# Optimization experiments

Hardware: AMD Instinct MI355X
Metric: run time of the kernel (lower is better)

The kernel has to match this reference:

```python
import jax, jax.numpy as jnp
import numpy as np

B, N, M, D, H = 2, 4096, 4096, 512, 8
P = D // H


def setup_inputs() -> dict:
    key = jax.random.key(0)
    ks = jax.random.split(key, 9)
    s = 1.0 / np.sqrt(D)
    return {
        "queries": jax.random.normal(ks[0], (B, N, D), dtype=jnp.float32),
        "keys": jax.random.normal(ks[1], (B, M, D), dtype=jnp.float32),
        "values": jax.random.normal(ks[2], (B, M, D), dtype=jnp.float32),
        "Wq": jax.random.normal(ks[3], (D, D), dtype=jnp.float32) * s,
        "bq": jax.random.normal(ks[4], (D,), dtype=jnp.float32) * s,
        "Wk": jax.random.normal(ks[5], (D, D), dtype=jnp.float32) * s,
        "bk": jax.random.normal(ks[6], (D,), dtype=jnp.float32) * s,
        "Wv": jax.random.normal(ks[7], (D, D), dtype=jnp.float32) * s,
        "bv": jax.random.normal(ks[8], (D,), dtype=jnp.float32) * s,
    }


def reference(queries, keys, values, Wq, bq, Wk, bk, Wv, bv):
    b, n, d = queries.shape
    m = keys.shape[1]
    h, p = H, D // H
    temperature = jnp.asarray(p, queries.dtype) ** 0.5
    # Linear projections (torch Linear: x @ W^T + b; here W stored as [in, out])
    q = (queries @ Wq + bq).reshape(b, n, h, p)
    k = (keys @ Wk + bk).reshape(b, m, h, p)
    v = (values @ Wv + bv).reshape(b, m, h, p)
    # scaled dot-product attention per head; scores [b, h, n, m]
    scores = jnp.einsum("bnhp,bmhp->bhnm", q, k) / temperature
    attn = jax.nn.softmax(scores, axis=-1)
    out = jnp.einsum("bhnm,bmhp->bnhp", attn, v)
    return out.reshape(b, n, d)
```

## Files before the change

### kernel.cpp

```cpp
#include <hip/hip_runtime.h>
#include <stdint.h>

#define B_ 2
#define N_ 4096
#define M_ 4096
#define D_ 512
#define H_ 8
#define P_ 64

typedef short bf16x8 __attribute__((ext_vector_type(8)));
typedef float f32x4 __attribute__((ext_vector_type(4)));
typedef unsigned short u16;
typedef unsigned int u32;
typedef u32 u32x4 __attribute__((ext_vector_type(4)));

static __device__ __forceinline__ u16 f2bf(float f) {
  u32 u = __builtin_bit_cast(u32, f);
  u32 r = u + 0x7fffu + ((u >> 16) & 1u);
  return (u16)(r >> 16);
}

static __device__ __forceinline__ u32 cvtpk(float lo, float hi_) {
  u32 d;
  asm("v_cvt_pk_bf16_f32 %0, %1, %2" : "=v"(d) : "v"(lo), "v"(hi_));
  return d;
}

static __device__ __forceinline__ float fexp2(float x) {
  float r;
  asm("v_exp_f32 %0, %1" : "=v"(r) : "v"(x));
  return r;
}

static __device__ __forceinline__ u32 permpk(const bf16x8& a0, const bf16x8& a1, int i) {
  u32x4 a0w = __builtin_bit_cast(u32x4, a0);
  u32x4 a1w = __builtin_bit_cast(u32x4, a1);
  int wd = i >> 1;
  u32 sel = (i & 1) ? 0x07060302u : 0x05040100u;
  return __builtin_amdgcn_perm(a1w[wd], a0w[wd], sel);
}

__global__ __launch_bounds__(256) void wt_kernel(const float* __restrict__ Wq,
                                                 const float* __restrict__ Wk,
                                                 const float* __restrict__ Wv,
                                                 u16* __restrict__ Wt) {
  __shared__ float tile[32][33];
  int z = blockIdx.z;
  const float* W = (z == 0) ? Wq : (z == 1) ? Wk : Wv;
  u16* out = Wt + (size_t)z * D_ * D_;
  int o0 = blockIdx.x * 32, d0 = blockIdx.y * 32;
  int tx = threadIdx.x, ty = threadIdx.y;
#pragma unroll
  for (int k = 0; k < 4; k++) tile[ty + k * 8][tx] = W[(size_t)(d0 + ty + k * 8) * D_ + o0 + tx];
  __syncthreads();
#pragma unroll
  for (int k = 0; k < 4; k++) out[(size_t)(o0 + ty + k * 8) * D_ + d0 + tx] = f2bf(tile[tx][ty + k * 8]);
}

__global__ __launch_bounds__(256) void proj_kernel(const float* __restrict__ Xq,
                                                   const float* __restrict__ Xk,
                                                   const float* __restrict__ Xv,
                                                   const u16* __restrict__ Wt,
                                                   const float* __restrict__ bq,
                                                   const float* __restrict__ bk,
                                                   const float* __restrict__ bv,
                                                   u16* __restrict__ QKV) {
  int z = blockIdx.z;
  const float* X = (z == 0) ? Xq : (z == 1) ? Xk : Xv;
  const float* bias = (z == 0) ? bq : (z == 1) ? bk : bv;
  const u16* W = Wt + (size_t)z * D_ * D_;
  u16* Y = QKV + (size_t)z * (B_ * N_ * D_);
  const float scale = (z == 0) ? 0.18033688011112042f : 1.0f;

  __shared__ u16 Alds[128 * 32];
  __shared__ u16 Blds[128 * 32];

  int t = threadIdx.x;
  int lane = t & 63, w = t >> 6;
  int wm = w >> 1, wn = w & 1;
  int l15 = lane & 15, g = lane >> 4;
  int rb = blockIdx.y * 128, ob = blockIdx.x * 128;

  const f32x4 zero4 = {0.f, 0.f, 0.f, 0.f};
  f32x4 acc[4][4];
#pragma unroll
  for (int m = 0; m < 4; m++)
#pragma unroll
    for (int n = 0; n < 4; n++) acc[m][n] = zero4;

  for (int kb = 0; kb < D_; kb += 32) {
    __syncthreads();
#pragma unroll
    for (int i = 0; i < 4; i++) {
      int chunk = t + i * 256;
      int row = chunk >> 3, c4 = chunk & 7;
      const float4 v = *(const float4*)&X[(size_t)(rb + row) * D_ + kb + c4 * 4];
      u32 lo = (u32)f2bf(v.x) | ((u32)f2bf(v.y) << 16);
      u32 hi = (u32)f2bf(v.z) | ((u32)f2bf(v.w) << 16);
      int byte = row * 64 + ((c4 * 8) ^ ((row & 3) << 4));
      uint2 d;
      d.x = lo;
      d.y = hi;
      *(uint2*)((char*)Alds + byte) = d;
    }
#pragma unroll
    for (int i = 0; i < 2; i++) {
      int chunk = t + i * 256;
      int row = chunk >> 2, c = chunk & 3;
      bf16x8 v = *(const bf16x8*)&W[(size_t)(ob + row) * D_ + kb + c * 8];
      int byte = row * 64 + ((c * 16) ^ ((row & 3) << 4));
      *(bf16x8*)((char*)Blds + byte) = v;
    }
    __syncthreads();

    bf16x8 a[4], b[4];
#pragma unroll
    for (int m = 0; m < 4; m++) {
      int row = wm * 64 + m * 16 + l15;
      int byte = row * 64 + ((g * 16) ^ ((row & 3) << 4));
      a[m] = *(const bf16x8*)((char*)Alds + byte);
    }
#pragma unroll
    for (int n = 0; n < 4; n++) {
      int row = wn * 64 + n * 16 + l15;
      int byte = row * 64 + ((g * 16) ^ ((row & 3) << 4));
      b[n] = *(const bf16x8*)((char*)Blds + byte);
    }
#pragma unroll
    for (int m = 0; m < 4; m++)
#pragma unroll
      for (int n = 0; n < 4; n++)
        acc[m][n] = __builtin_amdgcn_mfma_f32_16x16x32_bf16(a[m], b[n], acc[m][n], 0, 0, 0);
  }

#pragma unroll
  for (int n = 0; n < 4; n++) {
    int col = ob + wn * 64 + n * 16 + l15;
    float bv_ = bias[col];
#pragma unroll
    for (int m = 0; m < 4; m++) {
      int row0 = rb + wm * 64 + m * 16 + g * 4;
#pragma unroll
      for (int r = 0; r < 4; r++) {
        float y = (acc[m][n][r] + bv_) * scale;
        Y[(size_t)(row0 + r) * D_ + col] = f2bf(y);
      }
    }
  }
}

__global__ __launch_bounds__(256, 2) void attn_kernel(const u16* __restrict__ QKV,
                                                      float* __restrict__ out) {
  const u16* Q = QKV;
  const u16* K = QKV + (size_t)(B_ * N_ * D_);
  const u16* V = K + (size_t)(B_ * N_ * D_);

  __shared__ u16 Klds[2][128 * 64];
  __shared__ u16 Vlds[2][2][64 * 64];

  char* KL = (char*)&Klds[0][0];
  char* VL = (char*)&Vlds[0][0][0];

  int t = threadIdx.x, l = t & 63, w = t >> 6;
  int l15 = l & 15, g = (l >> 4) & 3;
  int swz = (l15 & 7) << 4;

  int bid = blockIdx.x + 32 * (blockIdx.y + 8 * blockIdx.z);
  int sbid = (bid & 7) * 64 + (bid >> 3);
  int qt = sbid & 31, h = (sbid >> 5) & 7, b = sbid >> 8;
  int qwa = qt * 128 + w * 16;
  int qwb = qwa + 64;

  const u16* Kb = K + (size_t)(b * M_) * D_ + h * P_;
  const u16* Vb = V + (size_t)(b * M_) * D_ + h * P_;

  bf16x8 qfa[2], qfb[2];
  const u16* qrow_a = Q + (size_t)(b * N_ + qwa + l15) * D_ + h * P_;
  const u16* qrow_b = Q + (size_t)(b * N_ + qwb + l15) * D_ + h * P_;
#pragma unroll
  for (int step = 0; step < 2; step++) {
    qfa[step] = *(const bf16x8*)(qrow_a + step * 32 + g * 8);
    qfb[step] = *(const bf16x8*)(qrow_b + step * 32 + g * 8);
  }

  int koff0 = l15 * 128 + ((g * 16) ^ swz);
  int koff1 = l15 * 128 + ((64 + g * 16) ^ swz);
  int voff0 = koff0, voff1 = koff1;
  int krow = t >> 3, kc = t & 7;
  int kwoff = krow * 128 + ((kc * 16) ^ ((krow & 7) << 4));
  const u16* kg = Kb + (size_t)krow * D_ + kc * 8;
  int kp = t & 31, p0 = (t >> 5) * 8;
  int kv0 = 2 * kp, blk = kv0 >> 5, ww_ = kv0 & 31;
  int slot = blk * 32 + ((ww_ >> 2) & 3) * 8 + ((ww_ >> 4) << 2) + (ww_ & 3);
  int vwB = p0 * 128 + 2 * slot;
  const u16* vg0 = Vb + (size_t)kv0 * D_ + p0;
  const u16* vg1 = vg0 + D_;

  const f32x4 zc = {0.f, 0.f, 0.f, 0.f};
  const u32x4 onesw = {0x3F803F80u, 0x3F803F80u, 0x3F803F80u, 0x3F803F80u};
  const bf16x8 ones_f = __builtin_bit_cast(bf16x8, onesw);
  f32x4 oa[4], ob_[4], ol_a = zc, ol_b = zc;
#pragma unroll
  for (int i = 0; i < 4; i++) {
    oa[i] = zc;
    ob_[i] = zc;
  }

  {
#pragma unroll
    for (int i = 0; i < 4; i++)
      *(bf16x8*)(KL + kwoff + i * 4096) = *(const bf16x8*)(kg + (size_t)(32 * i) * D_);
    bf16x8 a0 = *(const bf16x8*)vg0;
    bf16x8 a1 = *(const bf16x8*)vg1;
    bf16x8 c0 = *(const bf16x8*)(vg0 + (size_t)64 * D_);
    bf16x8 c1 = *(const bf16x8*)(vg1 + (size_t)64 * D_);
#pragma unroll
    for (int i = 0; i < 8; i++) {
      int off = (vwB ^ (i << 4)) + i * 128;
      *(u32*)(VL + off) = permpk(a0, a1, i);
      *(u32*)(VL + off + 8192) = permpk(c0, c1, i);
    }
  }
  kwoff ^= 0x4000;
  vwB ^= 0x4000;
  const u16* kgp = kg + (size_t)128 * D_;
  const u16* vgp0 = vg0 + (size_t)128 * D_;
  const u16* vgp1 = vg1 + (size_t)128 * D_;
  __syncthreads();

  const int NT = M_ / 128;
  for (int kt = 0; kt < NT; kt++) {
    bf16x8 kn0 = {}, kn1 = {}, kn2 = {}, kn3 = {}, vnA0 = {}, vnA1 = {}, vnB0 = {}, vnB1 = {};
    if (kt + 1 < NT) {
      kn0 = *(const bf16x8*)kgp;
      kn1 = *(const bf16x8*)(kgp + (size_t)32 * D_);
      kn2 = *(const bf16x8*)(kgp + (size_t)64 * D_);
      kn3 = *(const bf16x8*)(kgp + (size_t)96 * D_);
      vnA0 = *(const bf16x8*)vgp0;
      vnA1 = *(const bf16x8*)vgp1;
      vnB0 = *(const bf16x8*)(vgp0 + (size_t)64 * D_);
      vnB1 = *(const bf16x8*)(vgp1 + (size_t)64 * D_);
      kgp += (size_t)128 * D_;
      vgp0 += (size_t)128 * D_;
      vgp1 += (size_t)128 * D_;
    }

#pragma unroll
    for (int hh = 0; hh < 2; hh++) {
      const int hb = hh * 8192;

      f32x4 sa[4], sb[4];
      __builtin_amdgcn_s_setprio(1);
#pragma unroll
      for (int tt = 0; tt < 4; tt++) {
        bf16x8 kf0 = *(const bf16x8*)(KL + koff0 + hb + tt * 2048);
        sa[tt] = __builtin_amdgcn_mfma_f32_16x16x32_bf16(kf0, qfa[0], zc, 0, 0, 0);
        sb[tt] = __builtin_amdgcn_mfma_f32_16x16x32_bf16(kf0, qfb[0], zc, 0, 0, 0);
        bf16x8 kf1 = *(const bf16x8*)(KL + koff1 + hb + tt * 2048);
        sa[tt] = __builtin_amdgcn_mfma_f32_16x16x32_bf16(kf1, qfa[1], sa[tt], 0, 0, 0);
        sb[tt] = __builtin_amdgcn_mfma_f32_16x16x32_bf16(kf1, qfb[1], sb[tt], 0, 0, 0);
      }
      __builtin_amdgcn_s_setprio(0);

#pragma unroll
      for (int tt = 0; tt < 4; tt++)
#pragma unroll
        for (int r = 0; r < 4; r++) {
          sa[tt][r] = fexp2(sa[tt][r]);
          sb[tt][r] = fexp2(sb[tt][r]);
        }

      u32 pwa[2][4], pwb[2][4];
#pragma unroll
      for (int kb2 = 0; kb2 < 2; kb2++)
#pragma unroll
        for (int wd = 0; wd < 4; wd++) {
          const f32x4& sva = sa[2 * kb2 + (wd >> 1)];
          const f32x4& svb = sb[2 * kb2 + (wd >> 1)];
          pwa[kb2][wd] = cvtpk(sva[(wd & 1) * 2], sva[(wd & 1) * 2 + 1]);
          pwb[kb2][wd] = cvtpk(svb[(wd & 1) * 2], svb[(wd & 1) * 2 + 1]);
        }

      __builtin_amdgcn_s_setprio(1);
#pragma unroll
      for (int kb2 = 0; kb2 < 2; kb2++) {
        u32x4 pva = {pwa[kb2][0], pwa[kb2][1], pwa[kb2][2], pwa[kb2][3]};
        u32x4 pvb = {pwb[kb2][0], pwb[kb2][1], pwb[kb2][2], pwb[kb2][3]};
        bf16x8 pfa = __builtin_bit_cast(bf16x8, pva);
        bf16x8 pfb = __builtin_bit_cast(bf16x8, pvb);
        int voff = (kb2 ? voff1 : voff0) + hb;
#pragma unroll
        for (int tt = 0; tt < 4; tt++) {
          bf16x8 vf = *(const bf16x8*)(VL + voff + tt * 2048);
          oa[tt] = __builtin_amdgcn_mfma_f32_16x16x32_bf16(vf, pfa, oa[tt], 0, 0, 0);
          ob_[tt] = __builtin_amdgcn_mfma_f32_16x16x32_bf16(vf, pfb, ob_[tt], 0, 0, 0);
        }
        ol_a = __builtin_amdgcn_mfma_f32_16x16x32_bf16(ones_f, pfa, ol_a, 0, 0, 0);
        ol_b = __builtin_amdgcn_mfma_f32_16x16x32_bf16(ones_f, pfb, ol_b, 0, 0, 0);
      }
      __builtin_amdgcn_s_setprio(0);
    }

    if (kt + 1 < NT) {
      *(bf16x8*)(KL + kwoff) = kn0;
      *(bf16x8*)(KL + kwoff + 4096) = kn1;
      *(bf16x8*)(KL + kwoff + 8192) = kn2;
      *(bf16x8*)(KL + kwoff + 12288) = kn3;
#pragma unroll
      for (int i = 0; i < 8; i++) {
        int off = (vwB ^ (i << 4)) + i * 128;
        *(u32*)(VL + off) = permpk(vnA0, vnA1, i);
        *(u32*)(VL + off + 8192) = permpk(vnB0, vnB1, i);
      }
    }
    koff0 ^= 0x4000;
    koff1 ^= 0x4000;
    voff0 ^= 0x4000;
    voff1 ^= 0x4000;
    kwoff ^= 0x4000;
    vwB ^= 0x4000;
    __syncthreads();
  }

  float rla = 1.0f / ol_a[0], rlb = 1.0f / ol_b[0];
  float* orow_a = out + (size_t)(b * N_ + qwa + l15) * D_ + h * P_;
  float* orow_b = out + (size_t)(b * N_ + qwb + l15) * D_ + h * P_;
#pragma unroll
  for (int tt = 0; tt < 4; tt++) {
    float4 sta = {oa[tt][0] * rla, oa[tt][1] * rla, oa[tt][2] * rla, oa[tt][3] * rla};
    *(float4*)(orow_a + tt * 16 + g * 4) = sta;
    float4 stb = {ob_[tt][0] * rlb, ob_[tt][1] * rlb, ob_[tt][2] * rlb, ob_[tt][3] * rlb};
    *(float4*)(orow_b + tt * 16 + g * 4) = stb;
  }
}

extern "C" void kernel_launch(void* const* d_in, const int* in_sizes, int n_in,
                              void* d_out, int out_size, void* d_ws, size_t ws_size,
                              hipStream_t stream) {
  const float* queries = (const float*)d_in[0];
  const float* keys = (const float*)d_in[1];
  const float* values = (const float*)d_in[2];
  const float* Wq = (const float*)d_in[3];
  const float* bq = (const float*)d_in[4];
  const float* Wk = (const float*)d_in[5];
  const float* bk = (const float*)d_in[6];
  const float* Wv = (const float*)d_in[7];
  const float* bv = (const float*)d_in[8];
  float* out = (float*)d_out;

  u16* QKV = (u16*)d_ws;
  u16* Wt = QKV + (size_t)3 * B_ * N_ * D_;

  wt_kernel<<<dim3(16, 16, 3), dim3(32, 8), 0, stream>>>(Wq, Wk, Wv, Wt);
  proj_kernel<<<dim3(4, 64, 3), 256, 0, stream>>>(queries, keys, values, Wt, bq, bk, bv, QKV);
  attn_kernel<<<dim3(32, 8, 2), 256, 0, stream>>>(QKV, out);
}
```

Before: 120.8 us.

## Double attention query tile to 256 rows with 512-thread blocks sharing K/V tiles

The attention kernel now runs 8 waves per block over 256 query rows, so each staged 128-key K/V tile in LDS serves twice as many queries. Each thread loads half as many K/V vectors per iteration, which cuts global and LDS-staging traffic per query. The inner loop also computes scores for both 64-key halves before the exp and PV stages, giving the scheduler more independent MFMA work. The costs are higher register pressure under the tighter (512,2) launch bound, which could cause spills, and a grid half as large (256 blocks).

```diff
diff --git a/kernel.cpp b/kernel.cpp
--- a/kernel.cpp
+++ b/kernel.cpp
@@ -149,7 +149,7 @@
   }
 }
 
-__global__ __launch_bounds__(256, 2) void attn_kernel(const u16* __restrict__ QKV,
+__global__ __launch_bounds__(512, 2) void attn_kernel(const u16* __restrict__ QKV,
                                                       float* __restrict__ out) {
   const u16* Q = QKV;
   const u16* K = QKV + (size_t)(B_ * N_ * D_);
@@ -165,11 +165,11 @@
   int l15 = l & 15, g = (l >> 4) & 3;
   int swz = (l15 & 7) << 4;
 
-  int bid = blockIdx.x + 32 * (blockIdx.y + 8 * blockIdx.z);
-  int sbid = (bid & 7) * 64 + (bid >> 3);
-  int qt = sbid & 31, h = (sbid >> 5) & 7, b = sbid >> 8;
-  int qwa = qt * 128 + w * 16;
-  int qwb = qwa + 64;
+  int bid = blockIdx.x + 16 * (blockIdx.y + 8 * blockIdx.z);
+  int sbid = (bid & 7) * 32 + (bid >> 3);
+  int qt = sbid & 15, h = (sbid >> 4) & 7, b = sbid >> 7;
+  int qwa = qt * 256 + w * 16;
+  int qwb = qwa + 128;
 
   const u16* Kb = K + (size_t)(b * M_) * D_ + h * P_;
   const u16* Vb = V + (size_t)(b * M_) * D_ + h * P_;
@@ -186,14 +186,17 @@
   int koff0 = l15 * 128 + ((g * 16) ^ swz);
   int koff1 = l15 * 128 + ((64 + g * 16) ^ swz);
   int voff0 = koff0, voff1 = koff1;
+
   int krow = t >> 3, kc = t & 7;
   int kwoff = krow * 128 + ((kc * 16) ^ ((krow & 7) << 4));
-  const u16* kg = Kb + (size_t)krow * D_ + kc * 8;
-  int kp = t & 31, p0 = (t >> 5) * 8;
-  int kv0 = 2 * kp, blk = kv0 >> 5, ww_ = kv0 & 31;
-  int slot = blk * 32 + ((ww_ >> 2) & 3) * 8 + ((ww_ >> 4) << 2) + (ww_ & 3);
-  int vwB = p0 * 128 + 2 * slot;
-  const u16* vg0 = Vb + (size_t)kv0 * D_ + p0;
+  const u16* kg0 = Kb + (size_t)krow * D_ + kc * 8;
+  const u16* kg1 = kg0 + (size_t)64 * D_;
+  int hv = t >> 8, th = t & 255;
+  int kp = th & 31, p0 = (th >> 5) * 8;
+  int kv0 = 2 * kp, blk2 = kv0 >> 5, ww_ = kv0 & 31;
+  int slot = blk2 * 32 + ((ww_ >> 2) & 3) * 8 + ((ww_ >> 4) << 2) + (ww_ & 3);
+  int vwB = hv * 0x2000 + p0 * 128 + 2 * slot;
+  const u16* vg0 = Vb + (size_t)(hv * 64 + kv0) * D_ + p0;
   const u16* vg1 = vg0 + D_;
 
   const f32x4 zc = {0.f, 0.f, 0.f, 0.f};
@@ -207,111 +210,137 @@
   }
 
   {
-#pragma unroll
-    for (int i = 0; i < 4; i++)
-      *(bf16x8*)(KL + kwoff + i * 4096) = *(const bf16x8*)(kg + (size_t)(32 * i) * D_);
+    *(bf16x8*)(KL + kwoff) = *(const bf16x8*)kg0;
+    *(bf16x8*)(KL + kwoff + 8192) = *(const bf16x8*)kg1;
     bf16x8 a0 = *(const bf16x8*)vg0;
     bf16x8 a1 = *(const bf16x8*)vg1;
-    bf16x8 c0 = *(const bf16x8*)(vg0 + (size_t)64 * D_);
-    bf16x8 c1 = *(const bf16x8*)(vg1 + (size_t)64 * D_);
-#pragma unroll
-    for (int i = 0; i < 8; i++) {
-      int off = (vwB ^ (i << 4)) + i * 128;
-      *(u32*)(VL + off) = permpk(a0, a1, i);
-      *(u32*)(VL + off + 8192) = permpk(c0, c1, i);
-    }
+#pragma unroll
+    for (int i = 0; i < 8; i++) *(u32*)(VL + ((vwB ^ (i << 4)) + i * 128)) = permpk(a0, a1, i);
   }
   kwoff ^= 0x4000;
   vwB ^= 0x4000;
-  const u16* kgp = kg + (size_t)128 * D_;
+  const u16* kgp0 = kg0 + (size_t)128 * D_;
+  const u16* kgp1 = kg1 + (size_t)128 * D_;
   const u16* vgp0 = vg0 + (size_t)128 * D_;
   const u16* vgp1 = vg1 + (size_t)128 * D_;
   __syncthreads();
 
   const int NT = M_ / 128;
   for (int kt = 0; kt < NT; kt++) {
-    bf16x8 kn0 = {}, kn1 = {}, kn2 = {}, kn3 = {}, vnA0 = {}, vnA1 = {}, vnB0 = {}, vnB1 = {};
+    bf16x8 kn0 = {}, kn1 = {}, vn0 = {}, vn1 = {};
     if (kt + 1 < NT) {
-      kn0 = *(const bf16x8*)kgp;
-      kn1 = *(const bf16x8*)(kgp + (size_t)32 * D_);
-      kn2 = *(const bf16x8*)(kgp + (size_t)64 * D_);
-      kn3 = *(const bf16x8*)(kgp + (size_t)96 * D_);
-      vnA0 = *(const bf16x8*)vgp0;
-      vnA1 = *(const bf16x8*)vgp1;
-      vnB0 = *(const bf16x8*)(vgp0 + (size_t)64 * D_);
-      vnB1 = *(const bf16x8*)(vgp1 + (size_t)64 * D_);
-      kgp += (size_t)128 * D_;
+      kn0 = *(const bf16x8*)kgp0;
+      kn1 = *(const bf16x8*)kgp1;
+      vn0 = *(const bf16x8*)vgp0;
+      vn1 = *(const bf16x8*)vgp1;
+      kgp0 += (size_t)128 * D_;
+      kgp1 += (size_t)128 * D_;
       vgp0 += (size_t)128 * D_;
       vgp1 += (size_t)128 * D_;
     }
 
-#pragma unroll
-    for (int hh = 0; hh < 2; hh++) {
-      const int hb = hh * 8192;
-
-      f32x4 sa[4], sb[4];
-      __builtin_amdgcn_s_setprio(1);
+    f32x4 sa0[4], sb0[4], sa1[4], sb1[4];
+
+    __builtin_amdgcn_s_setprio(1);
+#pragma unroll
+    for (int tt = 0; tt < 4; tt++) {
+      bf16x8 kf0 = *(const bf16x8*)(KL + koff0 + tt * 2048);
+      sa0[tt] = __builtin_amdgcn_mfma_f32_16x16x32_bf16(kf0, qfa[0], zc, 0, 0, 0);
+      sb0[tt] = __builtin_amdgcn_mfma_f32_16x16x32_bf16(kf0, qfb[0], zc, 0, 0, 0);
+      bf16x8 kf1 = *(const bf16x8*)(KL + koff1 + tt * 2048);
+      sa0[tt] = __builtin_amdgcn_mfma_f32_16x16x32_bf16(kf1, qfa[1], sa0[tt], 0, 0, 0);
+      sb0[tt] = __builtin_amdgcn_mfma_f32_16x16x32_bf16(kf1, qfb[1], sb0[tt], 0, 0, 0);
+    }
+#pragma unroll
+    for (int tt = 0; tt < 4; tt++) {
+      bf16x8 kf0 = *(const bf16x8*)(KL + koff0 + 8192 + tt * 2048);
+      sa1[tt] = __builtin_amdgcn_mfma_f32_16x16x32_bf16(kf0, qfa[0], zc, 0, 0, 0);
+      sb1[tt] = __builtin_amdgcn_mfma_f32_16x16x32_bf16(kf0, qfb[0], zc, 0, 0, 0);
+      bf16x8 kf1 = *(const bf16x8*)(KL + koff1 + 8192 + tt * 2048);
+      sa1[tt] = __builtin_amdgcn_mfma_f32_16x16x32_bf16(kf1, qfa[1], sa1[tt], 0, 0, 0);
+      sb1[tt] = __builtin_amdgcn_mfma_f32_16x16x32_bf16(kf1, qfb[1], sb1[tt], 0, 0, 0);
+    }
+    __builtin_amdgcn_s_setprio(0);
+
+    u32 pwa0[2][4], pwb0[2][4];
+#pragma unroll
+    for (int tt = 0; tt < 4; tt++)
+#pragma unroll
+      for (int r = 0; r < 4; r++) {
+        sa0[tt][r] = fexp2(sa0[tt][r]);
+        sb0[tt][r] = fexp2(sb0[tt][r]);
+      }
+#pragma unroll
+    for (int kb2 = 0; kb2 < 2; kb2++)
+#pragma unroll
+      for (int wd = 0; wd < 4; wd++) {
+        const f32x4& sva = sa0[2 * kb2 + (wd >> 1)];
+        const f32x4& svb = sb0[2 * kb2 + (wd >> 1)];
+        pwa0[kb2][wd] = cvtpk(sva[(wd & 1) * 2], sva[(wd & 1) * 2 + 1]);
+        pwb0[kb2][wd] = cvtpk(svb[(wd & 1) * 2], svb[(wd & 1) * 2 + 1]);
+      }
+
+    __builtin_amdgcn_s_setprio(1);
+#pragma unroll
+    for (int kb2 = 0; kb2 < 2; kb2++) {
+      u32x4 pva = {pwa0[kb2][0], pwa0[kb2][1], pwa0[kb2][2], pwa0[kb2][3]};
+      u32x4 pvb = {pwb0[kb2][0], pwb0[kb2][1], pwb0[kb2][2], pwb0[kb2][3]};
+      bf16x8 pfa = __builtin_bit_cast(bf16x8, pva);
+      bf16x8 pfb = __builtin_bit_cast(bf16x8, pvb);
+      int voff = kb2 ? voff1 : voff0;
 #pragma unroll
       for (int tt = 0; tt < 4; tt++) {
-        bf16x8 kf0 = *(const bf16x8*)(KL + koff0 + hb + tt * 2048);
-        sa[tt] = __builtin_amdgcn_mfma_f32_16x16x32_bf16(kf0, qfa[0], zc, 0, 0, 0);
-        sb[tt] = __builtin_amdgcn_mfma_f32_16x16x32_bf16(kf0, qfb[0], zc, 0, 0, 0);
-        bf16x8 kf1 = *(const bf16x8*)(KL + koff1 + hb + tt * 2048);
-        sa[tt] = __builtin_amdgcn_mfma_f32_16x16x32_bf16(kf1, qfa[1], sa[tt], 0, 0, 0);
-        sb[tt] = __builtin_amdgcn_mfma_f32_16x16x32_bf16(kf1, qfb[1], sb[tt], 0, 0, 0);
-      }
-      __builtin_amdgcn_s_setprio(0);
-
-#pragma unroll
-      for (int tt = 0; tt < 4; tt++)
-#pragma unroll
-        for (int r = 0; r < 4; r++) {
-          sa[tt][r] = fexp2(sa[tt][r]);
-          sb[tt][r] = fexp2(sb[tt][r]);
-        }
-
-      u32 pwa[2][4], pwb[2][4];
-#pragma unroll
-      for (int kb2 = 0; kb2 < 2; kb2++)
-#pragma unroll
-        for (int wd = 0; wd < 4; wd++) {
-          const f32x4& sva = sa[2 * kb2 + (wd >> 1)];
-          const f32x4& svb = sb[2 * kb2 + (wd >> 1)];
-          pwa[kb2][wd] = cvtpk(sva[(wd & 1) * 2], sva[(wd & 1) * 2 + 1]);
-          pwb[kb2][wd] = cvtpk(svb[(wd & 1) * 2], svb[(wd & 1) * 2 + 1]);
-        }
-
-      __builtin_amdgcn_s_setprio(1);
-#pragma unroll
-      for (int kb2 = 0; kb2 < 2; kb2++) {
-        u32x4 pva = {pwa[kb2][0], pwa[kb2][1], pwa[kb2][2], pwa[kb2][3]};
-        u32x4 pvb = {pwb[kb2][0], pwb[kb2][1], pwb[kb2][2], pwb[kb2][3]};
-        bf16x8 pfa = __builtin_bit_cast(bf16x8, pva);
-        bf16x8 pfb = __builtin_bit_cast(bf16x8, pvb);
-        int voff = (kb2 ? voff1 : voff0) + hb;
-#pragma unroll
-        for (int tt = 0; tt < 4; tt++) {
-          bf16x8 vf = *(const bf16x8*)(VL + voff + tt * 2048);
-          oa[tt] = __builtin_amdgcn_mfma_f32_16x16x32_bf16(vf, pfa, oa[tt], 0, 0, 0);
-          ob_[tt] = __builtin_amdgcn_mfma_f32_16x16x32_bf16(vf, pfb, ob_[tt], 0, 0, 0);
-        }
-        ol_a = __builtin_amdgcn_mfma_f32_16x16x32_bf16(ones_f, pfa, ol_a, 0, 0, 0);
-        ol_b = __builtin_amdgcn_mfma_f32_16x16x32_bf16(ones_f, pfb, ol_b, 0, 0, 0);
-      }
-      __builtin_amdgcn_s_setprio(0);
-    }
+        bf16x8 vf = *(const bf16x8*)(VL + voff + tt * 2048);
+        oa[tt] = __builtin_amdgcn_mfma_f32_16x16x32_bf16(vf, pfa, oa[tt], 0, 0, 0);
+        ob_[tt] = __builtin_amdgcn_mfma_f32_16x16x32_bf16(vf, pfb, ob_[tt], 0, 0, 0);
+      }
+      ol_a = __builtin_amdgcn_mfma_f32_16x16x32_bf16(ones_f, pfa, ol_a, 0, 0, 0);
+      ol_b = __builtin_amdgcn_mfma_f32_16x16x32_bf16(ones_f, pfb, ol_b, 0, 0, 0);
+    }
+    __builtin_amdgcn_s_setprio(0);
+
+    u32 pwa1[2][4], pwb1[2][4];
+#pragma unroll
+    for (int tt = 0; tt < 4; tt++)
+#pragma unroll
+      for (int r = 0; r < 4; r++) {
+        sa1[tt][r] = fexp2(sa1[tt][r]);
+        sb1[tt][r] = fexp2(sb1[tt][r]);
+      }
+#pragma unroll
+    for (int kb2 = 0; kb2 < 2; kb2++)
+#pragma unroll
+      for (int wd = 0; wd < 4; wd++) {
+        const f32x4& sva = sa1[2 * kb2 + (wd >> 1)];
+        const f32x4& svb = sb1[2 * kb2 + (wd >> 1)];
+        pwa1[kb2][wd] = cvtpk(sva[(wd & 1) * 2], sva[(wd & 1) * 2 + 1]);
+        pwb1[kb2][wd] = cvtpk(svb[(wd & 1) * 2], svb[(wd & 1) * 2 + 1]);
+      }
+
+    __builtin_amdgcn_s_setprio(1);
+#pragma unroll
+    for (int kb2 = 0; kb2 < 2; kb2++) {
+      u32x4 pva = {pwa1[kb2][0], pwa1[kb2][1], pwa1[kb2][2], pwa1[kb2][3]};
+      u32x4 pvb = {pwb1[kb2][0], pwb1[kb2][1], pwb1[kb2][2], pwb1[kb2][3]};
+      bf16x8 pfa = __builtin_bit_cast(bf16x8, pva);
+      bf16x8 pfb = __builtin_bit_cast(bf16x8, pvb);
+      int voff = (kb2 ? voff1 : voff0) + 0x2000;
+#pragma unroll
+      for (int tt = 0; tt < 4; tt++) {
+        bf16x8 vf = *(const bf16x8*)(VL + voff + tt * 2048);
+        oa[tt] = __builtin_amdgcn_mfma_f32_16x16x32_bf16(vf, pfa, oa[tt], 0, 0, 0);
+        ob_[tt] = __builtin_amdgcn_mfma_f32_16x16x32_bf16(vf, pfb, ob_[tt], 0, 0, 0);
+      }
+      ol_a = __builtin_amdgcn_mfma_f32_16x16x32_bf16(ones_f, pfa, ol_a, 0, 0, 0);
+      ol_b = __builtin_amdgcn_mfma_f32_16x16x32_bf16(ones_f, pfb, ol_b, 0, 0, 0);
+    }
+    __builtin_amdgcn_s_setprio(0);
 
     if (kt + 1 < NT) {
       *(bf16x8*)(KL + kwoff) = kn0;
-      *(bf16x8*)(KL + kwoff + 4096) = kn1;
-      *(bf16x8*)(KL + kwoff + 8192) = kn2;
-      *(bf16x8*)(KL + kwoff + 12288) = kn3;
-#pragma unroll
-      for (int i = 0; i < 8; i++) {
-        int off = (vwB ^ (i << 4)) + i * 128;
-        *(u32*)(VL + off) = permpk(vnA0, vnA1, i);
-        *(u32*)(VL + off + 8192) = permpk(vnB0, vnB1, i);
-      }
+      *(bf16x8*)(KL + kwoff + 8192) = kn1;
+#pragma unroll
+      for (int i = 0; i < 8; i++) *(u32*)(VL + ((vwB ^ (i << 4)) + i * 128)) = permpk(vn0, vn1, i);
     }
     koff0 ^= 0x4000;
     koff1 ^= 0x4000;
@@ -353,5 +382,5 @@
 
   wt_kernel<<<dim3(16, 16, 3), dim3(32, 8), 0, stream>>>(Wq, Wk, Wv, Wt);
   proj_kernel<<<dim3(4, 64, 3), 256, 0, stream>>>(queries, keys, values, Wt, bq, bk, bv, QKV);
-  attn_kernel<<<dim3(32, 8, 2), 256, 0, stream>>>(QKV, out);
-}
+  attn_kernel<<<dim3(16, 8, 2), 512, 0, stream>>>(QKV, out);
+}
```

Result: faster. 114.1 us (-5.5%).
